# Kernel optimization log

Measured on AMD Instinct MI355X. Metric: run time of the kernel, lower is better.

The kernel has to match this reference:

```python
import jax, jax.numpy as jnp
import numpy as np

B, S, D = 8, 512, 768
HEADS = 16           # label_n
HD = 64              # size_per_head
NEG = 1e12


def setup_inputs() -> dict:
    key = jax.random.key(0)
    k1, k2, k3 = jax.random.split(key, 3)
    hidden = jax.random.normal(k1, (B, S, D), dtype=jnp.float32)
    token_ids = jax.random.randint(k2, (B, S), 0, 21128, dtype=jnp.int32)
    W = jax.random.normal(k3, (D, HEADS * 2 * HD), dtype=jnp.float32) * 0.02
    b = jnp.zeros((HEADS * 2 * HD,), dtype=jnp.float32)
    return {"hidden": hidden, "token_ids": token_ids, "W": W, "b": b}


def _rope(x):
    # x: [B, S, H, HD] -> RoPE-rotated, Su Jianlin interleaved convention
    d = x.shape[-1]
    inv_freq = 1.0 / (10000.0 ** (jnp.arange(0, d, 2, dtype=jnp.float32) / d))  # [d/2]
    pos = jnp.arange(x.shape[1], dtype=jnp.float32)                              # [S]
    freqs = pos[:, None] * inv_freq[None, :]                                     # [S, d/2]
    sin = jnp.repeat(jnp.sin(freqs), 2, axis=-1)[None, :, None, :]               # [1,S,1,d]
    cos = jnp.repeat(jnp.cos(freqs), 2, axis=-1)[None, :, None, :]
    x2 = jnp.stack([-x[..., 1::2], x[..., 0::2]], axis=-1).reshape(x.shape)
    return x * cos + x2 * sin


def reference(hidden, token_ids, W, b):
    # qk projection: [B,S,H,2,HD]
    qk = (hidden @ W + b).reshape(B, S, HEADS, 2, HD)
    q, k = qk[..., 0, :], qk[..., 1, :]          # [B,S,H,HD]
    q = _rope(q)
    k = _rope(k)
    # all-pairs span scores per entity head
    logits = jnp.einsum('bmhd,bnhd->bhmn', q, k) / jnp.sqrt(jnp.float32(HD))
    # padding mask from token ids (0 = pad)
    mask = (token_ids > 0).astype(logits.dtype)  # [B,S]
    logits = logits - (1.0 - mask[:, None, :, None]) * NEG
    logits = logits - (1.0 - mask[:, None, None, :]) * NEG
    # strict lower-triangular mask (spans must have start <= end)
    tril = jnp.tril(jnp.ones((S, S), dtype=logits.dtype), k=-1)
    logits = logits - tril[None, None, :, :] * NEG
    # valid-span weight mask (upper triangle incl. diag, both positions valid)
    tri_mask = (1.0 - tril)[None, None, :, :] * mask[:, None, :, None] * mask[:, None, None, :]
    return logits, tri_mask
```

## Files before the change

### kernel.cpp

```cpp
#include <hip/hip_runtime.h>
#include <hip/hip_bf16.h>
#include <cstdint>
#include <cstddef>


#define NEGV 1.0e12f

typedef short bf16x8 __attribute__((ext_vector_type(8)));
typedef float f32x4  __attribute__((ext_vector_type(4)));

static __device__ __forceinline__ short f2b(float x) {
    __hip_bfloat16 h = __float2bfloat16(x);
    union { __hip_bfloat16 h; short s; } u; u.h = h; return u.s;
}
static __device__ __forceinline__ float b2f(short s) {
    union { short s; __hip_bfloat16 h; } u; u.s = s; return __bfloat162float(u.h);
}
static __device__ __forceinline__ void gload16(const short* g, short* l) {
    __builtin_amdgcn_global_load_lds(
        (const __attribute__((address_space(1))) void*)g,
        (__attribute__((address_space(3))) void*)l, 16, 0, 0);
}

__global__ __launch_bounds__(256) void prep_kernel(const float* __restrict__ hidden,
                                                   const float* __restrict__ W,
                                                   short* __restrict__ Xb,
                                                   short* __restrict__ Wt,
                                                   float* __restrict__ SinT,
                                                   float* __restrict__ CosT) {
    __shared__ short T[64 * 68];
    int blk = blockIdx.x, tid = threadIdx.x;
    if (blk < 1536) {
        int t = blk * 256 + tid;
        const float4* hp = (const float4*)hidden;
        float4 a = hp[t * 2], c = hp[t * 2 + 1];
        bf16x8 v;
        v[0] = f2b(a.x); v[1] = f2b(a.y); v[2] = f2b(a.z); v[3] = f2b(a.w);
        v[4] = f2b(c.x); v[5] = f2b(c.y); v[6] = f2b(c.z); v[7] = f2b(c.w);
        *(bf16x8*)(Xb + t * 8) = v;
    } else if (blk < 1600) {
        int u = (blk - 1536) * 256 + tid;
        int s = u >> 5, i = u & 31;
        float ang = (float)s * exp2f(-0.4152410118609203f * (float)i);
        float sn, cs; __sincosf(ang, &sn, &cs);
        SinT[u] = sn; CosT[u] = cs;
    } else {
        int tb = blk - 1600;
        int k0 = (tb % 12) * 64, n0 = (tb / 12) * 64;
        int r = tid >> 2, cb = (tid & 3) * 4;
#pragma unroll
        for (int q = 0; q < 4; ++q) {
            int c = cb + q * 16;
            float4 v = *(const float4*)(W + (size_t)(k0 + r) * 2048 + n0 + c);
            short* tp = T + r * 68 + c;
            tp[0] = f2b(v.x); tp[1] = f2b(v.y); tp[2] = f2b(v.z); tp[3] = f2b(v.w);
        }
        __syncthreads();
        int n = tid >> 2, kc = (tid & 3) * 16;
        bf16x8 o0, o1;
#pragma unroll
        for (int j = 0; j < 8; ++j) {
            o0[j] = T[(kc + j) * 68 + n];
            o1[j] = T[(kc + 8 + j) * 68 + n];
        }
        short* wp = Wt + (size_t)(n0 + n) * 768 + k0 + kc;
        *(bf16x8*)wp = o0;
        *(bf16x8*)(wp + 8) = o1;
    }
}

__global__ __launch_bounds__(256) void gemm_rope(const short* __restrict__ A,
                                                 const short* __restrict__ Bt,
                                                 const float* __restrict__ bias,
                                                 const float* __restrict__ SinT,
                                                 const float* __restrict__ CosT,
                                                 short* __restrict__ Qb,
                                                 short* __restrict__ Kb) {
    __shared__ short As[2][128 * 32];
    __shared__ short Bs[2][128 * 32];
    const int m0 = (blockIdx.x >> 4) * 128;
    const int n0 = (blockIdx.x & 15) * 128;
    const int tid  = threadIdx.x;
    const int wave = tid >> 6, lane = tid & 63;
    const int quad = lane >> 4, r16 = lane & 15;
    const int wm = (wave >> 1) * 64, wn = (wave & 1) * 64;

    const int swc = ((lane & 3) ^ ((lane >> 3) & 3)) * 8;
    const int r0  = wave * 32 + (lane >> 2);
    const short* gA0 = A  + (size_t)(m0 + r0) * 768 + swc;
    const short* gA1 = A  + (size_t)(m0 + r0 + 16) * 768 + swc;
    const short* gB0 = Bt + (size_t)(n0 + r0) * 768 + swc;
    const short* gB1 = Bt + (size_t)(n0 + r0 + 16) * 768 + swc;
    const int stg = wave * 1024;

    const int sw16 = (r16 >> 1) & 3;

    gload16(gA0, As[0] + stg);
    gload16(gA1, As[0] + stg + 512);
    gload16(gB0, Bs[0] + stg);
    gload16(gB1, Bs[0] + stg + 512);

    f32x4 acc[4][4] = {};
#pragma unroll 2
    for (int t = 0; t < 24; ++t) {
        const int cur = t & 1;
        __syncthreads();
        if (t + 1 < 24) {
            const int k1 = (t + 1) * 32;
            gload16(gA0 + k1, As[cur ^ 1] + stg);
            gload16(gA1 + k1, As[cur ^ 1] + stg + 512);
            gload16(gB0 + k1, Bs[cur ^ 1] + stg);
            gload16(gB1 + k1, Bs[cur ^ 1] + stg + 512);
        }
        const short* Ab = As[cur];
        const short* Bb = Bs[cur];
        bf16x8 af[4], bfr[4];
#pragma unroll
        for (int mi = 0; mi < 4; ++mi)
            af[mi] = *(const bf16x8*)(Ab + (wm + mi * 16 + r16) * 32 + (quad ^ sw16) * 8);
#pragma unroll
        for (int ni = 0; ni < 4; ++ni)
            bfr[ni] = *(const bf16x8*)(Bb + (wn + ni * 16 + r16) * 32 + (quad ^ sw16) * 8);
#pragma unroll
        for (int mi = 0; mi < 4; ++mi)
#pragma unroll
            for (int ni = 0; ni < 4; ++ni)
                acc[mi][ni] = __builtin_amdgcn_mfma_f32_16x16x32_bf16(
                    af[mi], bfr[ni], acc[mi][ni], 0, 0, 0);
    }

    const int b     = m0 >> 9;
    const int s0l   = (m0 & 511) + wm + quad * 4;
    const int h     = n0 >> 7;
    const int which = wn >> 6;
    short* dstT = (which ? Kb : Qb) + (size_t)(b * 16 + h) * 512 * 64;
    const float sgn = (r16 & 1) ? 1.0f : -1.0f;
#pragma unroll
    for (int ni = 0; ni < 4; ++ni) {
        int col = n0 + wn + ni * 16 + r16;
        float bv = bias[col];
        int d  = ni * 16 + r16;
        int ii = d >> 1;
#pragma unroll
        for (int mi = 0; mi < 4; ++mi)
#pragma unroll
            for (int r = 0; r < 4; ++r) {
                int s = s0l + mi * 16 + r;
                float v  = acc[mi][ni][r] + bv;
                float pv = __shfl_xor(v, 1);
                float sn = SinT[s * 32 + ii];
                float cs = CosT[s * 32 + ii];
                dstT[(size_t)s * 64 + d] = f2b(v * cs + sgn * pv * sn);
            }
    }
}

__global__ __launch_bounds__(256) void logits_kernel(const short* __restrict__ Qb,
                                                     const short* __restrict__ Kb,
                                                     const int* __restrict__ tok,
                                                     float* __restrict__ out,
                                                     float* __restrict__ out2) {
    __shared__ short Qs[128 * 64];
    __shared__ short Ks[128 * 64];
    __shared__ float rowNeg[128];
    __shared__ float colNeg[128];

    int blk = blockIdx.x;
    int nt = blk & 3, mt = (blk >> 2) & 3, bh = blk >> 4;
    int b = bh >> 4, h = bh & 15;
    int m0 = mt * 128, n0 = nt * 128;

    const int tid  = threadIdx.x;
    const int wave = tid >> 6, lane = tid & 63;
    const int quad = lane >> 4, r16 = lane & 15;
    const int wm = (wave >> 1) * 64, wn = (wave & 1) * 64;

    const short* gsrc = (wave < 2)
        ? Qb + ((size_t)bh * 512 + m0) * 64
        : Kb + ((size_t)bh * 512 + n0) * 64;
    short* ldst = (wave < 2) ? Qs : Ks;
    const int wv = wave & 1;
    const int gc = ((lane & 7) ^ (lane >> 3)) * 8;
    const int rl = wv * 64 + (lane >> 3);
#pragma unroll
    for (int j = 0; j < 8; ++j)
        gload16(gsrc + (rl + j * 8) * 64 + gc, ldst + wv * 4096 + j * 512);

    if (tid < 128)      rowNeg[tid]       = (tok[b * 512 + m0 + tid] > 0) ? 0.f : NEGV;
    else if (tid < 256) colNeg[tid - 128] = (tok[b * 512 + n0 + (tid - 128)] > 0) ? 0.f : NEGV;
    __syncthreads();

    const int sw8 = r16 & 7;
    f32x4 acc[4][4] = {};
#pragma unroll
    for (int kb = 0; kb < 2; ++kb) {
        bf16x8 af[4], bfr[4];
#pragma unroll
        for (int mi = 0; mi < 4; ++mi)
            af[mi] = *(const bf16x8*)(Qs + (wm + mi * 16 + r16) * 64
                                         + ((quad + kb * 4) ^ sw8) * 8);
#pragma unroll
        for (int ni = 0; ni < 4; ++ni)
            bfr[ni] = *(const bf16x8*)(Ks + (wn + ni * 16 + r16) * 64
                                          + ((quad + kb * 4) ^ sw8) * 8);
#pragma unroll
        for (int mi = 0; mi < 4; ++mi)
#pragma unroll
            for (int ni = 0; ni < 4; ++ni)
                acc[mi][ni] = __builtin_amdgcn_mfma_f32_16x16x32_bf16(
                    af[mi], bfr[ni], acc[mi][ni], 0, 0, 0);
    }

    float* obase = out + (size_t)bh * 512 * 512;
#pragma unroll
    for (int mi = 0; mi < 4; ++mi)
#pragma unroll
        for (int ni = 0; ni < 4; ++ni) {
            int n = n0 + wn + ni * 16 + r16;
            float cn = colNeg[n - n0];
#pragma unroll
            for (int r = 0; r < 4; ++r) {
                int m = m0 + wm + mi * 16 + quad * 4 + r;
                float v = acc[mi][ni][r] * 0.125f - rowNeg[m - m0] - cn
                          - ((m > n) ? NEGV : 0.0f);
                obase[(size_t)m * 512 + n] = v;
            }
        }

    if (h == 0) {
        float* o2 = out2 + (size_t)b * 512 * 512;
#pragma unroll
        for (int mi = 0; mi < 4; ++mi)
#pragma unroll
            for (int ni = 0; ni < 4; ++ni) {
                int n = n0 + wn + ni * 16 + r16;
                float mn = (colNeg[n - n0] == 0.f) ? 1.f : 0.f;
#pragma unroll
                for (int r = 0; r < 4; ++r) {
                    int m = m0 + wm + mi * 16 + quad * 4 + r;
                    float mm = (rowNeg[m - m0] == 0.f) ? 1.f : 0.f;
                    o2[(size_t)m * 512 + n] = (m > n) ? 0.f : (mm * mn);
                }
            }
    }
}

extern "C" void kernel_launch(void* const* d_in, const int* in_sizes, int n_in,
                              void* d_out, int out_size, void* d_ws, size_t ws_size,
                              hipStream_t stream) {
    const float* hidden = (const float*)d_in[0];
    const int*   tok    = (const int*)d_in[1];
    const float* W      = (const float*)d_in[2];
    const float* bias   = (const float*)d_in[3];
    float* out  = (float*)d_out;
    float* out2 = out + 33554432;

    char* ws = (char*)d_ws;
    short* Xb   = (short*)(ws);
    short* Wt   = (short*)(ws + 6291456);
    float* SinT = (float*)(ws + 9437184);
    float* CosT = (float*)(ws + 9502720);
    short* Qb   = (short*)(ws + 9568256);
    short* Kb   = (short*)(ws + 17956864);

    hipLaunchKernelGGL(prep_kernel,   dim3(1984), dim3(256), 0, stream,
                       hidden, W, Xb, Wt, SinT, CosT);
    hipLaunchKernelGGL(gemm_rope,     dim3(512),  dim3(256), 0, stream,
                       Xb, Wt, bias, SinT, CosT, Qb, Kb);
    hipLaunchKernelGGL(logits_kernel, dim3(2048), dim3(256), 0, stream,
                       Qb, Kb, tok, out, out2);
}
```

Before: 193.7 us.

## Replace double-buffered GEMM staging with single buffer and remap blocks across XCDs

The projection GEMM drops its double-buffered LDS prefetch and instead loads each K-slice into a single buffer, with a barrier before and after the load. Both the GEMM and the logits kernels now remap blockIdx so that consecutive logical tiles go to the same XCD (stride-8 interleave), aiming for better L2 locality of the shared A/B and Q/K tiles. Halving LDS may raise occupancy. In exchange, the global-to-LDS load latency is no longer overlapped with the MFMA work within a block.

```diff
diff --git a/kernel.cpp b/kernel.cpp
--- a/kernel.cpp
+++ b/kernel.cpp
@@ -76,10 +76,11 @@
                                                  const float* __restrict__ CosT,
                                                  short* __restrict__ Qb,
                                                  short* __restrict__ Kb) {
-    __shared__ short As[2][128 * 32];
-    __shared__ short Bs[2][128 * 32];
-    const int m0 = (blockIdx.x >> 4) * 128;
-    const int n0 = (blockIdx.x & 15) * 128;
+    __shared__ short As[128 * 32];
+    __shared__ short Bs[128 * 32];
+    const int blk = (blockIdx.x & 7) * 64 + (blockIdx.x >> 3);
+    const int m0 = (blk >> 4) * 128;
+    const int n0 = (blk & 15) * 128;
     const int tid  = threadIdx.x;
     const int wave = tid >> 6, lane = tid & 63;
     const int quad = lane >> 4, r16 = lane & 15;
@@ -91,36 +92,29 @@
     const short* gA1 = A  + (size_t)(m0 + r0 + 16) * 768 + swc;
     const short* gB0 = Bt + (size_t)(n0 + r0) * 768 + swc;
     const short* gB1 = Bt + (size_t)(n0 + r0 + 16) * 768 + swc;
-    const int stg = wave * 1024;
+    short* lA0 = As + wave * 1024;
+    short* lA1 = As + wave * 1024 + 512;
+    short* lB0 = Bs + wave * 1024;
+    short* lB1 = Bs + wave * 1024 + 512;
 
     const int sw16 = (r16 >> 1) & 3;
 
-    gload16(gA0, As[0] + stg);
-    gload16(gA1, As[0] + stg + 512);
-    gload16(gB0, Bs[0] + stg);
-    gload16(gB1, Bs[0] + stg + 512);
-
     f32x4 acc[4][4] = {};
-#pragma unroll 2
-    for (int t = 0; t < 24; ++t) {
-        const int cur = t & 1;
+    for (int k0 = 0; k0 < 768; k0 += 32) {
         __syncthreads();
-        if (t + 1 < 24) {
-            const int k1 = (t + 1) * 32;
-            gload16(gA0 + k1, As[cur ^ 1] + stg);
-            gload16(gA1 + k1, As[cur ^ 1] + stg + 512);
-            gload16(gB0 + k1, Bs[cur ^ 1] + stg);
-            gload16(gB1 + k1, Bs[cur ^ 1] + stg + 512);
-        }
-        const short* Ab = As[cur];
-        const short* Bb = Bs[cur];
+        gload16(gA0 + k0, lA0);
+        gload16(gA1 + k0, lA1);
+        gload16(gB0 + k0, lB0);
+        gload16(gB1 + k0, lB1);
+        __syncthreads();
+
         bf16x8 af[4], bfr[4];
 #pragma unroll
         for (int mi = 0; mi < 4; ++mi)
-            af[mi] = *(const bf16x8*)(Ab + (wm + mi * 16 + r16) * 32 + (quad ^ sw16) * 8);
+            af[mi] = *(const bf16x8*)(As + (wm + mi * 16 + r16) * 32 + (quad ^ sw16) * 8);
 #pragma unroll
         for (int ni = 0; ni < 4; ++ni)
-            bfr[ni] = *(const bf16x8*)(Bb + (wn + ni * 16 + r16) * 32 + (quad ^ sw16) * 8);
+            bfr[ni] = *(const bf16x8*)(Bs + (wn + ni * 16 + r16) * 32 + (quad ^ sw16) * 8);
 #pragma unroll
         for (int mi = 0; mi < 4; ++mi)
 #pragma unroll
@@ -165,7 +159,7 @@
     __shared__ float rowNeg[128];
     __shared__ float colNeg[128];
 
-    int blk = blockIdx.x;
+    int blk = (blockIdx.x & 7) * 256 + (blockIdx.x >> 3);
     int nt = blk & 3, mt = (blk >> 2) & 3, bh = blk >> 4;
     int b = bh >> 4, h = bh & 15;
     int m0 = mt * 128, n0 = nt * 128;
```

Measured after the change: 190.1 us. Within noise of the previous version (-1.9%).
